# Performance work log

Hardware: AMD Instinct MI355X
Metric: run time of the kernel (lower is better)

The kernel has to match this reference:

```python
import jax, jax.numpy as jnp
import numpy as np

D_MODEL = 768
D_ATTN = 768
D_LLM = 4096
N_HEADS = 12
HEAD_DIM = D_ATTN // N_HEADS


def setup_inputs() -> dict:
    key = jax.random.key(0)
    ks = jax.random.split(key, 11)
    B, L, S = 8, 1024, 1000
    inp = {
        "target_embedding": jax.random.normal(ks[0], (B, L, D_MODEL), jnp.float32),
        "source_embedding": jax.random.normal(ks[1], (S, D_LLM), jnp.float32),
        "value_embedding": jax.random.normal(ks[2], (S, D_LLM), jnp.float32),
        # nn.Linear params: y = x @ W.T + b, W shape (out, in)
        "Wq": jax.random.normal(ks[3], (D_ATTN, D_MODEL), jnp.float32) * (1.0 / np.sqrt(D_MODEL)),
        "bq": jax.random.normal(ks[4], (D_ATTN,), jnp.float32) * 0.02,
        "Wk": jax.random.normal(ks[5], (D_ATTN, D_LLM), jnp.float32) * (1.0 / np.sqrt(D_LLM)),
        "bk": jax.random.normal(ks[6], (D_ATTN,), jnp.float32) * 0.02,
        "Wv": jax.random.normal(ks[7], (D_ATTN, D_LLM), jnp.float32) * (1.0 / np.sqrt(D_LLM)),
        "bv": jax.random.normal(ks[8], (D_ATTN,), jnp.float32) * 0.02,
        "Wo": jax.random.normal(ks[9], (D_LLM, D_ATTN), jnp.float32) * (1.0 / np.sqrt(D_ATTN)),
        "bo": jax.random.normal(ks[10], (D_LLM,), jnp.float32) * 0.02,
    }
    return inp


def reference(target_embedding, source_embedding, value_embedding,
              Wq, bq, Wk, bk, Wv, bv, Wo, bo):
    B, L, _ = target_embedding.shape
    S, _ = source_embedding.shape
    H, E = N_HEADS, HEAD_DIM
    scale = E ** -0.5

    q = (target_embedding @ Wq.T + bq).reshape(B, L, H, E)   # (B,L,H,E)
    k = (source_embedding @ Wk.T + bk).reshape(S, H, E)      # (S,H,E) shared KV
    v = (value_embedding @ Wv.T + bv).reshape(S, H, E)

    scores = jnp.einsum('blhe,she->bhls', q, k) * scale      # (B,H,L,S)
    A = jax.nn.softmax(scores, axis=-1)                      # dropout inactive (eval)
    rep = jnp.einsum('bhls,she->blhe', A, v).reshape(B, L, D_ATTN)
    return rep @ Wo.T + bo                                   # (B,L,D_LLM)
```

## Files before the change

### kernel.cpp

```cpp
#include <hip/hip_runtime.h>

typedef __attribute__((ext_vector_type(8))) short short8;
typedef __attribute__((ext_vector_type(4))) float f32x4;
typedef __attribute__((ext_vector_type(2))) unsigned u32x2;

#define DEVI __device__ __forceinline__

DEVI unsigned short f2bf(float x) {
  unsigned u = __builtin_bit_cast(unsigned, x);
  u += 0x7fff + ((u >> 16) & 1u);
  return (unsigned short)(u >> 16);
}

DEVI unsigned pkbf2(float a, float b) {
  return (unsigned)f2bf(a) | ((unsigned)f2bf(b) << 16);
}

__global__ __launch_bounds__(256) void cvt_all(
    const float* __restrict__ t0, const float* __restrict__ t1,
    const float* __restrict__ t2, const float* __restrict__ t3,
    const float* __restrict__ t4, const float* __restrict__ t5,
    const float* __restrict__ t6,
    unsigned short* __restrict__ o0, unsigned short* __restrict__ o1,
    unsigned short* __restrict__ o2, unsigned short* __restrict__ o3,
    unsigned short* __restrict__ o4, unsigned short* __restrict__ o5,
    unsigned short* __restrict__ o6) {
  const unsigned gid = blockIdx.x * 256 + threadIdx.x;
  const float* src;
  unsigned short* dst;
  unsigned base;
  if (gid < 786432u)       { src = t0; dst = o0; base = 0u; }
  else if (gid < 1298432u) { src = t1; dst = o1; base = 786432u; }
  else if (gid < 1810432u) { src = t2; dst = o2; base = 1298432u; }
  else if (gid < 1884160u) { src = t3; dst = o3; base = 1810432u; }
  else if (gid < 2277376u) { src = t4; dst = o4; base = 1884160u; }
  else if (gid < 2670592u) { src = t5; dst = o5; base = 2277376u; }
  else                     { src = t6; dst = o6; base = 2670592u; }
  const size_t i = (size_t)(gid - base) * 8;
  f32x4 a = *(const f32x4*)(src + i);
  f32x4 b = *(const f32x4*)(src + i + 4);
  short8 p;
#pragma unroll
  for (int j = 0; j < 4; ++j) p[j] = (short)f2bf(a[j]);
#pragma unroll
  for (int j = 0; j < 4; ++j) p[j + 4] = (short)f2bf(b[j]);
  *(short8*)&dst[i] = p;
}

template <int TM, int MODE>
DEVI void gemm_body(const unsigned short* __restrict__ A,
                    const unsigned short* __restrict__ B,
                    const float* __restrict__ bias, void* __restrict__ outp,
                    int M, int lda, int ldo, float scale,
                    int bm, int bn, int kbeg, int kend) {
  constexpr int WM = TM / 32;
  constexpr int ROWS = TM + 128;
  constexpr int NCH = ROWS / 16;
  constexpr int CPW = NCH / 4;
  __shared__ unsigned short sAB[ROWS * 32];
  const int tid = threadIdx.x;
  const int lane = tid & 63, wid = tid >> 6;
  const int wr = (wid >> 1) * (WM * 16), wc = (wid & 1) * 64;
  const int m0 = bm * TM, n0 = bn * 128;
  const int grow = lane >> 2, gcol = (lane & 3) * 8;
  const int lr = lane & 15, lk = (lane >> 4) * 8;

  f32x4 acc[WM][4];
#pragma unroll
  for (int i = 0; i < WM; ++i)
#pragma unroll
    for (int j = 0; j < 4; ++j) acc[i][j] = (f32x4){0.f, 0.f, 0.f, 0.f};

  for (int k0 = kbeg; k0 < kend; k0 += 32) {
#pragma unroll
    for (int i = 0; i < CPW; ++i) {
      const int c = wid * CPW + i;
      const int row = c * 16 + grow;
      const unsigned short* src;
      if (c * 16 < TM) {
        int rg = m0 + row;
        if (rg > M - 1) rg = M - 1;
        src = A + (size_t)rg * lda + k0 + gcol;
      } else {
        src = B + (size_t)(n0 + row - TM) * lda + k0 + gcol;
      }
      __builtin_amdgcn_global_load_lds(
          (const __attribute__((address_space(1))) unsigned int*)src,
          (__attribute__((address_space(3))) unsigned int*)(sAB + c * 512),
          16, 0, 0);
    }
    __syncthreads();
    short8 af[WM], bfr[4];
#pragma unroll
    for (int i = 0; i < WM; ++i) af[i]  = *(const short8*)&sAB[(wr + i * 16 + lr) * 32 + lk];
#pragma unroll
    for (int j = 0; j < 4; ++j)  bfr[j] = *(const short8*)&sAB[(TM + wc + j * 16 + lr) * 32 + lk];
#pragma unroll
    for (int i = 0; i < WM; ++i)
#pragma unroll
      for (int j = 0; j < 4; ++j)
        acc[i][j] = __builtin_amdgcn_mfma_f32_16x16x32_bf16(af[i], bfr[j], acc[i][j], 0, 0, 0);
    __syncthreads();
  }

#pragma unroll
  for (int i = 0; i < WM; ++i) {
#pragma unroll
    for (int j = 0; j < 4; ++j) {
      const int n  = n0 + wc + j * 16 + lr;
      const int mb = m0 + wr + i * 16 + (lane >> 4) * 4;
      if (MODE == 0) {
        const float bv = bias[n];
        unsigned short* out = (unsigned short*)outp;
#pragma unroll
        for (int r = 0; r < 4; ++r)
          out[(size_t)(mb + r) * ldo + n] = f2bf((acc[i][j][r] + bv) * scale);
      } else if (MODE == 1) {
        const float bv = bias[n];
        float* out = (float*)outp;
#pragma unroll
        for (int r = 0; r < 4; ++r)
          out[(size_t)(mb + r) * ldo + n] = acc[i][j][r] + bv;
      } else {
        float* out = (float*)outp;
#pragma unroll
        for (int r = 0; r < 4; ++r)
          out[(size_t)(mb + r) * ldo + n] = acc[i][j][r];
      }
    }
  }
}

__global__ __launch_bounds__(256) void qproj_kernel(const unsigned short* __restrict__ A,
                                                    const unsigned short* __restrict__ B,
                                                    const float* __restrict__ bq,
                                                    unsigned short* __restrict__ qb) {
  gemm_body<64, 0>(A, B, bq, qb, 8192, 768, 768, 0.18033688011112042f,
                   blockIdx.x, blockIdx.y, 0, 768);
}

__global__ __launch_bounds__(256) void kvproj_kernel(const unsigned short* __restrict__ sb,
                                                     const unsigned short* __restrict__ vb,
                                                     const unsigned short* __restrict__ wkb,
                                                     const unsigned short* __restrict__ wvb,
                                                     float* __restrict__ parts) {
  const int mat = blockIdx.z >> 2, ks = blockIdx.z & 3;
  const unsigned short* A = mat ? vb : sb;
  const unsigned short* B = mat ? wvb : wkb;
  float* out = parts + (size_t)blockIdx.z * 786432;
  gemm_body<64, 2>(A, B, nullptr, out, 1000, 4096, 768, 1.0f,
                   blockIdx.x, blockIdx.y, ks * 1024, ks * 1024 + 1024);
}

__global__ __launch_bounds__(256) void oproj_kernel(const unsigned short* __restrict__ A,
                                                    const unsigned short* __restrict__ B,
                                                    const float* __restrict__ bo,
                                                    float* __restrict__ out) {
  gemm_body<128, 1>(A, B, bo, out, 8192, 768, 4096, 1.0f,
                    blockIdx.x, blockIdx.y, 0, 768);
}

__global__ __launch_bounds__(256) void finalize_kv(const float* __restrict__ parts,
                                                   const float* __restrict__ bk,
                                                   const float* __restrict__ bv,
                                                   unsigned short* __restrict__ kb,
                                                   unsigned short* __restrict__ vtb) {
  if (blockIdx.z == 0) {
    const int i = (blockIdx.x * 256 + threadIdx.x) * 8;
    const int col = i % 768;
    f32x4 sa = (f32x4){0.f, 0.f, 0.f, 0.f}, sb = sa;
#pragma unroll
    for (int p = 0; p < 4; ++p) {
      sa += *(const f32x4*)(parts + (size_t)p * 786432 + i);
      sb += *(const f32x4*)(parts + (size_t)p * 786432 + i + 4);
    }
    short8 o;
#pragma unroll
    for (int j = 0; j < 4; ++j) o[j] = (short)f2bf(sa[j] + bk[col + j]);
#pragma unroll
    for (int j = 0; j < 4; ++j) o[j + 4] = (short)f2bf(sb[j] + bk[col + 4 + j]);
    *(short8*)&kb[i] = o;
  } else {
    const int idx = blockIdx.x * 256 + threadIdx.x;
    const int n = idx >> 7;
    const int s0 = (idx & 127) * 8;
    const float bvn = bv[n];
    short8 o;
#pragma unroll
    for (int j = 0; j < 8; ++j) {
      float s = 0.f;
#pragma unroll
      for (int p = 0; p < 4; ++p)
        s += parts[(size_t)(4 + p) * 786432 + (size_t)(s0 + j) * 768 + n];
      o[j] = (short)f2bf(s + bvn);
    }
    *(short8*)&vtb[(size_t)n * 1024 + s0] = o;
  }
}

__global__ __launch_bounds__(256) void attn_kernel(const unsigned short* __restrict__ q,
                                                   const unsigned short* __restrict__ k,
                                                   const unsigned short* __restrict__ vt,
                                                   unsigned short* __restrict__ rep) {
  __shared__ unsigned short sK[64][72];
  __shared__ unsigned short sV[64][72];
  __shared__ unsigned short sP[128][72];

  const int tid = threadIdx.x;
  const int lane = tid & 63, w = tid >> 6;
  const int g = lane >> 4;
  const int q0 = blockIdx.x * 128;
  const int b = blockIdx.y / 12, h = blockIdx.y % 12;
  const int lr = lane & 15, lk = g * 8;
  const int qrow_base = b * 1024 + q0 + w * 32;

  short8 qf[2][2];
#pragma unroll
  for (int fm = 0; fm < 2; ++fm)
#pragma unroll
    for (int kk = 0; kk < 2; ++kk)
      qf[fm][kk] = *(const short8*)&q[(size_t)(qrow_base + fm * 16 + lr) * 768 + h * 64 + kk * 32 + lk];

  float m_run[2] = {-1e30f, -1e30f};
  float l_run[2] = {0.f, 0.f};
  f32x4 o[2][4];
#pragma unroll
  for (int fm = 0; fm < 2; ++fm)
#pragma unroll
    for (int je = 0; je < 4; ++je) o[fm][je] = (f32x4){0.f, 0.f, 0.f, 0.f};

  const int strow = tid >> 2, stc = (tid & 3) * 16;

  for (int t = 0; t < 16; ++t) {
    const int s0 = t * 64;
    __syncthreads();
    {
      const unsigned short* ks = &k[(size_t)(s0 + strow) * 768 + h * 64 + stc];
      *(short8*)&sK[strow][stc]     = *(const short8*)ks;
      *(short8*)&sK[strow][stc + 8] = *(const short8*)(ks + 8);
      const unsigned short* vs = &vt[(size_t)(h * 64 + strow) * 1024 + s0 + stc];
      *(short8*)&sV[strow][stc]     = *(const short8*)vs;
      *(short8*)&sV[strow][stc + 8] = *(const short8*)(vs + 8);
    }
    __syncthreads();

    f32x4 sc[2][4];
#pragma unroll
    for (int fm = 0; fm < 2; ++fm)
#pragma unroll
      for (int j = 0; j < 4; ++j) sc[fm][j] = (f32x4){0.f, 0.f, 0.f, 0.f};
    short8 kf[4][2];
#pragma unroll
    for (int j = 0; j < 4; ++j)
#pragma unroll
      for (int kk = 0; kk < 2; ++kk)
        kf[j][kk] = *(const short8*)&sK[j * 16 + lr][kk * 32 + lk];
#pragma unroll
    for (int fm = 0; fm < 2; ++fm)
#pragma unroll
      for (int j = 0; j < 4; ++j)
#pragma unroll
        for (int kk = 0; kk < 2; ++kk)
          sc[fm][j] = __builtin_amdgcn_mfma_f32_16x16x32_bf16(kf[j][kk], qf[fm][kk], sc[fm][j], 0, 0, 0);

    if (s0 + 64 > 1000) {
#pragma unroll
      for (int j = 0; j < 4; ++j)
#pragma unroll
        for (int r = 0; r < 4; ++r)
          if (s0 + j * 16 + g * 4 + r >= 1000) {
            sc[0][j][r] = -1e30f;
            sc[1][j][r] = -1e30f;
          }
    }

    float fac[2];
#pragma unroll
    for (int fm = 0; fm < 2; ++fm) {
      float mx = -1e30f;
#pragma unroll
      for (int j = 0; j < 4; ++j) {
        float a = fmaxf(fmaxf(sc[fm][j][0], sc[fm][j][1]),
                        fmaxf(sc[fm][j][2], sc[fm][j][3]));
        mx = fmaxf(mx, a);
      }
      mx = fmaxf(mx, __shfl_xor(mx, 16));
      mx = fmaxf(mx, __shfl_xor(mx, 32));
      const float mnew = fmaxf(m_run[fm], mx);
      fac[fm] = exp2f(m_run[fm] - mnew);
      m_run[fm] = mnew;
      float rs = 0.f;
#pragma unroll
      for (int j = 0; j < 4; ++j)
#pragma unroll
        for (int r = 0; r < 4; ++r) {
          const float p = exp2f(sc[fm][j][r] - mnew);
          sc[fm][j][r] = p;
          rs += p;
        }
      rs += __shfl_xor(rs, 16);
      rs += __shfl_xor(rs, 32);
      l_run[fm] = l_run[fm] * fac[fm] + rs;
    }

#pragma unroll
    for (int fm = 0; fm < 2; ++fm)
#pragma unroll
      for (int r = 0; r < 4; ++r) {
        const float fq = __shfl(fac[fm], g * 20 + r);
#pragma unroll
        for (int je = 0; je < 4; ++je) o[fm][je][r] *= fq;
      }

#pragma unroll
    for (int fm = 0; fm < 2; ++fm)
#pragma unroll
      for (int j = 0; j < 4; ++j) {
        u32x2 pw;
        pw[0] = pkbf2(sc[fm][j][0], sc[fm][j][1]);
        pw[1] = pkbf2(sc[fm][j][2], sc[fm][j][3]);
        *(u32x2*)&sP[w * 32 + fm * 16 + lr][j * 16 + g * 4] = pw;
      }
    asm volatile("s_waitcnt lgkmcnt(0)" ::: "memory");

    short8 pf[2][2], vf[4][2];
#pragma unroll
    for (int fm = 0; fm < 2; ++fm)
#pragma unroll
      for (int kk = 0; kk < 2; ++kk)
        pf[fm][kk] = *(const short8*)&sP[w * 32 + fm * 16 + lr][kk * 32 + lk];
#pragma unroll
    for (int je = 0; je < 4; ++je)
#pragma unroll
      for (int kk = 0; kk < 2; ++kk)
        vf[je][kk] = *(const short8*)&sV[je * 16 + lr][kk * 32 + lk];
#pragma unroll
    for (int fm = 0; fm < 2; ++fm)
#pragma unroll
      for (int je = 0; je < 4; ++je)
#pragma unroll
        for (int kk = 0; kk < 2; ++kk)
          o[fm][je] = __builtin_amdgcn_mfma_f32_16x16x32_bf16(pf[fm][kk], vf[je][kk], o[fm][je], 0, 0, 0);
  }

#pragma unroll
  for (int fm = 0; fm < 2; ++fm) {
    const float il = 1.0f / l_run[fm];
#pragma unroll
    for (int r = 0; r < 4; ++r) {
      const float iq = __shfl(il, g * 20 + r);
#pragma unroll
      for (int je = 0; je < 4; ++je)
        sP[w * 32 + fm * 16 + g * 4 + r][je * 16 + lr] = f2bf(o[fm][je][r] * iq);
    }
  }
  __syncthreads();
  const int orow = tid >> 1, oc = (tid & 1) * 32;
  unsigned short* dst = &rep[(size_t)(b * 1024 + q0 + orow) * 768 + h * 64 + oc];
#pragma unroll
  for (int i = 0; i < 4; ++i)
    *(short8*)(dst + i * 8) = *(const short8*)&sP[orow][oc + i * 8];
}

extern "C" void kernel_launch(void* const* d_in, const int* in_sizes, int n_in,
                              void* d_out, int out_size, void* d_ws, size_t ws_size,
                              hipStream_t stream) {
  const float* target = (const float*)d_in[0];
  const float* source = (const float*)d_in[1];
  const float* value  = (const float*)d_in[2];
  const float* Wq = (const float*)d_in[3];
  const float* bq = (const float*)d_in[4];
  const float* Wk = (const float*)d_in[5];
  const float* bk = (const float*)d_in[6];
  const float* Wv = (const float*)d_in[7];
  const float* bv = (const float*)d_in[8];
  const float* Wo = (const float*)d_in[9];
  const float* bo = (const float*)d_in[10];
  float* out = (float*)d_out;

  char* ws = (char*)d_ws;
  unsigned short* qb   = (unsigned short*)(ws);
  unsigned short* kb   = (unsigned short*)(ws + 12582912);
  unsigned short* vtb  = (unsigned short*)(ws + 14155776);
  unsigned short* repb = (unsigned short*)(ws + 15728640);
  unsigned short* wob  = (unsigned short*)(ws + 28311552);

  char* ob = (char*)d_out;
  unsigned short* targetb = (unsigned short*)(ob);
  unsigned short* sourceb = (unsigned short*)(ob + 12582912);
  unsigned short* valueb  = (unsigned short*)(ob + 20774912);
  unsigned short* wqb     = (unsigned short*)(ob + 28966912);
  unsigned short* wkb     = (unsigned short*)(ob + 30146560);
  unsigned short* wvb     = (unsigned short*)(ob + 36438016);
  float* parts            = (float*)(ob + 42729472);

  cvt_all<<<11968, 256, 0, stream>>>(target, source, value, Wq, Wk, Wv, Wo,
                                     targetb, sourceb, valueb, wqb, wkb, wvb, wob);
  qproj_kernel<<<dim3(128, 6), 256, 0, stream>>>(targetb, wqb, bq, qb);
  kvproj_kernel<<<dim3(16, 6, 8), 256, 0, stream>>>(sourceb, valueb, wkb, wvb, parts);
  finalize_kv<<<dim3(384, 1, 2), 256, 0, stream>>>(parts, bk, bv, kb, vtb);
  attn_kernel<<<dim3(8, 96), 256, 0, stream>>>(qb, kb, vtb, repb);
  oproj_kernel<<<dim3(64, 32), 256, 0, stream>>>(repb, wob, bo, out);
}
```

Baseline: 448.2 us.

## Shrink attention tiles to 64 queries, swizzle LDS, lazily rescale softmax

The attention kernel now gives each block 64 query rows (16 per wave) instead of 128 and doubles the grid, with launch bounds asking for 4 blocks per CU. The padded shared tiles become XOR-swizzled 64x64 layouts to avoid bank conflicts, bf16 packing uses the hardware v_cvt_pk_bf16_f32 instruction, and the online-softmax rescale of the output accumulators is skipped unless the max grows by more than a threshold. The aim is better occupancy and less LDS and ALU overhead per tile. In exchange, each block reloads K/V tiles for fewer queries, which doubles K/V traffic into shared memory, and the lazy rescale relies on exp2 staying bounded when the max is stale.

```diff
diff --git a/kernel.cpp b/kernel.cpp
--- a/kernel.cpp
+++ b/kernel.cpp
@@ -12,8 +12,17 @@
   return (unsigned short)(u >> 16);
 }
 
-DEVI unsigned pkbf2(float a, float b) {
-  return (unsigned)f2bf(a) | ((unsigned)f2bf(b) << 16);
+DEVI unsigned cvtpk(float a, float b) {
+  unsigned r;
+  asm("v_cvt_pk_bf16_f32 %0, %1, %2" : "=v"(r) : "v"(a), "v"(b));
+  return r;
+}
+
+DEVI unsigned short* swz(unsigned short* base, int row, int colb) {
+  return (unsigned short*)((char*)base + row * 128 + (colb ^ ((row & 7) << 4)));
+}
+DEVI const unsigned short* swzc(const unsigned short* base, int row, int colb) {
+  return (const unsigned short*)((const char*)base + row * 128 + (colb ^ ((row & 7) << 4)));
 }
 
 __global__ __launch_bounds__(256) void cvt_all(
@@ -198,168 +207,134 @@
   }
 }
 
-__global__ __launch_bounds__(256) void attn_kernel(const unsigned short* __restrict__ q,
-                                                   const unsigned short* __restrict__ k,
-                                                   const unsigned short* __restrict__ vt,
-                                                   unsigned short* __restrict__ rep) {
-  __shared__ unsigned short sK[64][72];
-  __shared__ unsigned short sV[64][72];
-  __shared__ unsigned short sP[128][72];
+__global__ __launch_bounds__(256, 4) void attn_kernel(const unsigned short* __restrict__ q,
+                                                      const unsigned short* __restrict__ k,
+                                                      const unsigned short* __restrict__ vt,
+                                                      unsigned short* __restrict__ rep) {
+  __shared__ unsigned short sK[64 * 64];
+  __shared__ unsigned short sV[64 * 64];
+  __shared__ unsigned short sP[64 * 64];
 
   const int tid = threadIdx.x;
   const int lane = tid & 63, w = tid >> 6;
-  const int g = lane >> 4;
-  const int q0 = blockIdx.x * 128;
+  const int g = lane >> 4, lr = lane & 15;
+  const int q0 = blockIdx.x * 64;
   const int b = blockIdx.y / 12, h = blockIdx.y % 12;
-  const int lr = lane & 15, lk = g * 8;
-  const int qrow_base = b * 1024 + q0 + w * 32;
-
-  short8 qf[2][2];
-#pragma unroll
-  for (int fm = 0; fm < 2; ++fm)
-#pragma unroll
-    for (int kk = 0; kk < 2; ++kk)
-      qf[fm][kk] = *(const short8*)&q[(size_t)(qrow_base + fm * 16 + lr) * 768 + h * 64 + kk * 32 + lk];
-
-  float m_run[2] = {-1e30f, -1e30f};
-  float l_run[2] = {0.f, 0.f};
-  f32x4 o[2][4];
-#pragma unroll
-  for (int fm = 0; fm < 2; ++fm)
-#pragma unroll
-    for (int je = 0; je < 4; ++je) o[fm][je] = (f32x4){0.f, 0.f, 0.f, 0.f};
-
-  const int strow = tid >> 2, stc = (tid & 3) * 16;
+  const int qrow = b * 1024 + q0 + w * 16 + lr;
+
+  short8 qf[2];
+#pragma unroll
+  for (int kk = 0; kk < 2; ++kk)
+    qf[kk] = *(const short8*)&q[(size_t)qrow * 768 + h * 64 + kk * 32 + g * 8];
+
+  float m_run = -1e30f, l_run = 0.f;
+  f32x4 o[4];
+#pragma unroll
+  for (int je = 0; je < 4; ++je) o[je] = (f32x4){0.f, 0.f, 0.f, 0.f};
+
+  const int strow = tid >> 2;
+  const int stcb = (tid & 3) * 32;
 
   for (int t = 0; t < 16; ++t) {
     const int s0 = t * 64;
     __syncthreads();
     {
-      const unsigned short* ks = &k[(size_t)(s0 + strow) * 768 + h * 64 + stc];
-      *(short8*)&sK[strow][stc]     = *(const short8*)ks;
-      *(short8*)&sK[strow][stc + 8] = *(const short8*)(ks + 8);
-      const unsigned short* vs = &vt[(size_t)(h * 64 + strow) * 1024 + s0 + stc];
-      *(short8*)&sV[strow][stc]     = *(const short8*)vs;
-      *(short8*)&sV[strow][stc + 8] = *(const short8*)(vs + 8);
+      const unsigned short* ks = &k[(size_t)(s0 + strow) * 768 + h * 64 + (tid & 3) * 16];
+      *(short8*)swz(sK, strow, stcb)      = *(const short8*)ks;
+      *(short8*)swz(sK, strow, stcb + 16) = *(const short8*)(ks + 8);
+      const unsigned short* vs = &vt[(size_t)(h * 64 + strow) * 1024 + s0 + (tid & 3) * 16];
+      *(short8*)swz(sV, strow, stcb)      = *(const short8*)vs;
+      *(short8*)swz(sV, strow, stcb + 16) = *(const short8*)(vs + 8);
     }
     __syncthreads();
 
-    f32x4 sc[2][4];
-#pragma unroll
-    for (int fm = 0; fm < 2; ++fm)
-#pragma unroll
-      for (int j = 0; j < 4; ++j) sc[fm][j] = (f32x4){0.f, 0.f, 0.f, 0.f};
-    short8 kf[4][2];
+    f32x4 sc[4];
+#pragma unroll
+    for (int j = 0; j < 4; ++j) sc[j] = (f32x4){0.f, 0.f, 0.f, 0.f};
+#pragma unroll
+    for (int j = 0; j < 4; ++j) {
+#pragma unroll
+      for (int kk = 0; kk < 2; ++kk) {
+        const short8 kf = *(const short8*)swzc(sK, j * 16 + lr, kk * 64 + g * 16);
+        sc[j] = __builtin_amdgcn_mfma_f32_16x16x32_bf16(kf, qf[kk], sc[j], 0, 0, 0);
+      }
+    }
+
+    if (s0 + 64 > 1000) {
+#pragma unroll
+      for (int j = 0; j < 4; ++j)
+#pragma unroll
+        for (int r = 0; r < 4; ++r)
+          if (s0 + j * 16 + g * 4 + r >= 1000) sc[j][r] = -1e30f;
+    }
+
+    float mx = -1e30f;
 #pragma unroll
     for (int j = 0; j < 4; ++j)
-#pragma unroll
-      for (int kk = 0; kk < 2; ++kk)
-        kf[j][kk] = *(const short8*)&sK[j * 16 + lr][kk * 32 + lk];
-#pragma unroll
-    for (int fm = 0; fm < 2; ++fm)
-#pragma unroll
-      for (int j = 0; j < 4; ++j)
-#pragma unroll
-        for (int kk = 0; kk < 2; ++kk)
-          sc[fm][j] = __builtin_amdgcn_mfma_f32_16x16x32_bf16(kf[j][kk], qf[fm][kk], sc[fm][j], 0, 0, 0);
-
-    if (s0 + 64 > 1000) {
-#pragma unroll
-      for (int j = 0; j < 4; ++j)
-#pragma unroll
-        for (int r = 0; r < 4; ++r)
-          if (s0 + j * 16 + g * 4 + r >= 1000) {
-            sc[0][j][r] = -1e30f;
-            sc[1][j][r] = -1e30f;
-          }
-    }
-
-    float fac[2];
-#pragma unroll
-    for (int fm = 0; fm < 2; ++fm) {
-      float mx = -1e30f;
-#pragma unroll
-      for (int j = 0; j < 4; ++j) {
-        float a = fmaxf(fmaxf(sc[fm][j][0], sc[fm][j][1]),
-                        fmaxf(sc[fm][j][2], sc[fm][j][3]));
-        mx = fmaxf(mx, a);
-      }
-      mx = fmaxf(mx, __shfl_xor(mx, 16));
-      mx = fmaxf(mx, __shfl_xor(mx, 32));
-      const float mnew = fmaxf(m_run[fm], mx);
-      fac[fm] = exp2f(m_run[fm] - mnew);
-      m_run[fm] = mnew;
-      float rs = 0.f;
-#pragma unroll
-      for (int j = 0; j < 4; ++j)
-#pragma unroll
-        for (int r = 0; r < 4; ++r) {
-          const float p = exp2f(sc[fm][j][r] - mnew);
-          sc[fm][j][r] = p;
-          rs += p;
-        }
-      rs += __shfl_xor(rs, 16);
-      rs += __shfl_xor(rs, 32);
-      l_run[fm] = l_run[fm] * fac[fm] + rs;
-    }
-
-#pragma unroll
-    for (int fm = 0; fm < 2; ++fm)
+      mx = fmaxf(mx, fmaxf(fmaxf(sc[j][0], sc[j][1]), fmaxf(sc[j][2], sc[j][3])));
+    mx = fmaxf(mx, __shfl_xor(mx, 16));
+    mx = fmaxf(mx, __shfl_xor(mx, 32));
+    if (!__all(mx <= m_run + 8.0f)) {
+      const float mnew = fmaxf(m_run, mx);
+      const float fac = exp2f(m_run - mnew);
+      m_run = mnew;
+      l_run *= fac;
 #pragma unroll
       for (int r = 0; r < 4; ++r) {
-        const float fq = __shfl(fac[fm], g * 20 + r);
-#pragma unroll
-        for (int je = 0; je < 4; ++je) o[fm][je][r] *= fq;
-      }
-
-#pragma unroll
-    for (int fm = 0; fm < 2; ++fm)
-#pragma unroll
-      for (int j = 0; j < 4; ++j) {
-        u32x2 pw;
-        pw[0] = pkbf2(sc[fm][j][0], sc[fm][j][1]);
-        pw[1] = pkbf2(sc[fm][j][2], sc[fm][j][3]);
-        *(u32x2*)&sP[w * 32 + fm * 16 + lr][j * 16 + g * 4] = pw;
-      }
+        const float fq = __shfl(fac, g * 20 + r);
+#pragma unroll
+        for (int je = 0; je < 4; ++je) o[je][r] *= fq;
+      }
+    }
+    float rs = 0.f;
+#pragma unroll
+    for (int j = 0; j < 4; ++j)
+#pragma unroll
+      for (int r = 0; r < 4; ++r) {
+        const float p = exp2f(sc[j][r] - m_run);
+        sc[j][r] = p;
+        rs += p;
+      }
+    rs += __shfl_xor(rs, 16);
+    rs += __shfl_xor(rs, 32);
+    l_run += rs;
+
+#pragma unroll
+    for (int j = 0; j < 4; ++j) {
+      u32x2 pw;
+      pw[0] = cvtpk(sc[j][0], sc[j][1]);
+      pw[1] = cvtpk(sc[j][2], sc[j][3]);
+      *(u32x2*)swz(sP, w * 16 + lr, j * 32 + g * 8) = pw;
+    }
     asm volatile("s_waitcnt lgkmcnt(0)" ::: "memory");
 
-    short8 pf[2][2], vf[4][2];
-#pragma unroll
-    for (int fm = 0; fm < 2; ++fm)
-#pragma unroll
-      for (int kk = 0; kk < 2; ++kk)
-        pf[fm][kk] = *(const short8*)&sP[w * 32 + fm * 16 + lr][kk * 32 + lk];
+    short8 pf[2];
+#pragma unroll
+    for (int kk = 0; kk < 2; ++kk)
+      pf[kk] = *(const short8*)swzc(sP, w * 16 + lr, kk * 64 + g * 16);
+#pragma unroll
+    for (int je = 0; je < 4; ++je) {
+#pragma unroll
+      for (int kk = 0; kk < 2; ++kk) {
+        const short8 vf = *(const short8*)swzc(sV, je * 16 + lr, kk * 64 + g * 16);
+        o[je] = __builtin_amdgcn_mfma_f32_16x16x32_bf16(pf[kk], vf, o[je], 0, 0, 0);
+      }
+    }
+  }
+
+  const float il = 1.0f / l_run;
+#pragma unroll
+  for (int r = 0; r < 4; ++r) {
+    const float iq = __shfl(il, g * 20 + r);
 #pragma unroll
     for (int je = 0; je < 4; ++je)
-#pragma unroll
-      for (int kk = 0; kk < 2; ++kk)
-        vf[je][kk] = *(const short8*)&sV[je * 16 + lr][kk * 32 + lk];
-#pragma unroll
-    for (int fm = 0; fm < 2; ++fm)
-#pragma unroll
-      for (int je = 0; je < 4; ++je)
-#pragma unroll
-        for (int kk = 0; kk < 2; ++kk)
-          o[fm][je] = __builtin_amdgcn_mfma_f32_16x16x32_bf16(pf[fm][kk], vf[je][kk], o[fm][je], 0, 0, 0);
-  }
-
-#pragma unroll
-  for (int fm = 0; fm < 2; ++fm) {
-    const float il = 1.0f / l_run[fm];
-#pragma unroll
-    for (int r = 0; r < 4; ++r) {
-      const float iq = __shfl(il, g * 20 + r);
-#pragma unroll
-      for (int je = 0; je < 4; ++je)
-        sP[w * 32 + fm * 16 + g * 4 + r][je * 16 + lr] = f2bf(o[fm][je][r] * iq);
-    }
+      *swz(sP, w * 16 + g * 4 + r, (je * 16 + lr) * 2) = f2bf(o[je][r] * iq);
   }
   __syncthreads();
-  const int orow = tid >> 1, oc = (tid & 1) * 32;
-  unsigned short* dst = &rep[(size_t)(b * 1024 + q0 + orow) * 768 + h * 64 + oc];
-#pragma unroll
-  for (int i = 0; i < 4; ++i)
-    *(short8*)(dst + i * 8) = *(const short8*)&sP[orow][oc + i * 8];
+  const int orow = tid >> 2, ocb = (tid & 3) * 32;
+  unsigned short* dst = &rep[(size_t)(b * 1024 + q0 + orow) * 768 + h * 64 + (tid & 3) * 16];
+  *(short8*)dst       = *(const short8*)swzc(sP, orow, ocb);
+  *(short8*)(dst + 8) = *(const short8*)swzc(sP, orow, ocb + 16);
 }
 
 extern "C" void kernel_launch(void* const* d_in, const int* in_sizes, int n_in,
@@ -399,6 +374,6 @@
   qproj_kernel<<<dim3(128, 6), 256, 0, stream>>>(targetb, wqb, bq, qb);
   kvproj_kernel<<<dim3(16, 6, 8), 256, 0, stream>>>(sourceb, valueb, wkb, wvb, parts);
   finalize_kv<<<dim3(384, 1, 2), 256, 0, stream>>>(parts, bk, bv, kb, vtb);
-  attn_kernel<<<dim3(8, 96), 256, 0, stream>>>(qb, kb, vtb, repb);
+  attn_kernel<<<dim3(16, 96), 256, 0, stream>>>(qb, kb, vtb, repb);
   oproj_kernel<<<dim3(64, 32), 256, 0, stream>>>(repb, wob, bo, out);
 }
```

Result: faster. 418.5 us (-6.6%).
